# Optimization experiments

Hardware: AMD Instinct MI355X
Metric: run time of the kernel (lower is better)

Reference implementation:

```python
import jax, jax.numpy as jnp
import numpy as np

H = 256  # hidden_dim


def _bidir_lstm_layer(x, W_ih, W_hh, bias):
    """x: [S, B, in]; W_ih: [2, in, 4H]; W_hh: [2, H, 4H]; bias: [2, 4H].
    Returns [S, B, 2H] (forward || backward outputs per timestep).
    PyTorch gate order: i, f, g, o."""
    B = x.shape[1]
    init = (jnp.zeros((B, H), x.dtype), jnp.zeros((B, H), x.dtype))
    # precompute input projections for the whole sequence, both directions
    xp = jnp.einsum('sbi,dij->dsbj', x, W_ih) + bias[:, None, None, :]  # [2,S,B,4H]

    def make_step(W_hh_d):
        def step(carry, xt):
            h, c = carry
            g = xt + h @ W_hh_d  # [B, 4H]
            i = jax.nn.sigmoid(g[:, :H])
            f = jax.nn.sigmoid(g[:, H:2 * H])
            gg = jnp.tanh(g[:, 2 * H:3 * H])
            o = jax.nn.sigmoid(g[:, 3 * H:])
            c = f * c + i * gg
            h = o * jnp.tanh(c)
            return (h, c), h
        return step

    _, h_f = jax.lax.scan(make_step(W_hh[0]), init, xp[0])
    _, h_b = jax.lax.scan(make_step(W_hh[1]), init, xp[1], reverse=True)
    return jnp.concatenate([h_f, h_b], axis=-1)  # [S, B, 2H]


def setup_inputs() -> dict:
    key = jax.random.key(0)
    ks = jax.random.split(key, 11)
    s = 0.05  # small init scale to keep gates in their dynamic range
    inp = {
        'x': jax.random.normal(ks[0], (8192, 1024), jnp.float32),
        'w_ih0': jax.random.normal(ks[1], (2, 1024, 4 * H), jnp.float32) * s,
        'w_hh0': jax.random.normal(ks[2], (2, H, 4 * H), jnp.float32) * s,
        'b0': jax.random.normal(ks[3], (2, 4 * H), jnp.float32) * s,
        'w_ih': jax.random.normal(ks[4], (4, 2, 2 * H, 4 * H), jnp.float32) * s,
        'w_hh': jax.random.normal(ks[5], (4, 2, H, 4 * H), jnp.float32) * s,
        'b': jax.random.normal(ks[6], (4, 2, 4 * H), jnp.float32) * s,
        'w1': jax.random.normal(ks[7], (2 * H, 32), jnp.float32) * s,
        'b1': jax.random.normal(ks[8], (32,), jnp.float32) * s,
        'w2': jax.random.normal(ks[9], (32, 2), jnp.float32) * s,
        'b2': jax.random.normal(ks[10], (2,), jnp.float32) * s,
    }
    return inp


def reference(x, w_ih0, w_hh0, b0, w_ih, w_hh, b, w1, b1, w2, b2):
    # x: [S, 1024] -> [S, B=1, 1024] (module does unsqueeze(0).transpose(0,1))
    h = x[:, None, :]
    h = _bidir_lstm_layer(h, w_ih0, w_hh0, b0)
    for l in range(4):  # layers 1..4 (fixed count)
        h = _bidir_lstm_layer(h, w_ih[l], w_hh[l], b[l])
    # cat(forward output at last step, backward output at first step)
    feat = jnp.concatenate([h[-1, :, :H], h[0, :, H:]], axis=1)  # [1, 2H]
    out = (feat @ w1 + b1) @ w2 + b2  # [1, 2]
    return out
```

## Files before the change

kernel.cpp:

```cpp
#include <hip/hip_runtime.h>

constexpr int SQ = 8192;
constexpr int HD = 256;
constexpr int NG = 1024;

typedef __fp16 h2 __attribute__((ext_vector_type(2)));
typedef __fp16 f16x8 __attribute__((ext_vector_type(8)));
typedef float f32x4 __attribute__((ext_vector_type(4)));
typedef unsigned int uint;
typedef unsigned short ushort;

__device__ __forceinline__ float sigm_f(float x) {
  float e = __builtin_amdgcn_exp2f(-1.4426950408889634f * x);
  return __builtin_amdgcn_rcpf(1.0f + e);
}
__device__ __forceinline__ float tanh_f(float x) {
  float e = __builtin_amdgcn_exp2f(2.885390081777927f * x);
  return 1.0f - 2.0f * __builtin_amdgcn_rcpf(1.0f + e);
}
__device__ __forceinline__ h2 bch2(uint v) { return __builtin_bit_cast(h2, v); }
__device__ __forceinline__ uint pk(float a, float b) {
  return __builtin_bit_cast(uint, __builtin_amdgcn_cvt_pkrtz(a, b));
}
__device__ __forceinline__ f16x8 bcf(uint4 v) { return __builtin_bit_cast(f16x8, v); }
__device__ __forceinline__ float dpp_xor1(float x) {
  int v = __builtin_amdgcn_mov_dpp(__builtin_bit_cast(int, x), 0xB1, 0xF, 0xF, true);
  return __builtin_bit_cast(float, v);
}

__global__ __launch_bounds__(256) void gemm_mfma(const float* __restrict__ A, int K,
                                                 const float* __restrict__ W,
                                                 const float* __restrict__ bias,
                                                 float* __restrict__ out) {
  __shared__ __fp16 Ahi[64][40];
  __shared__ __fp16 Alo[64][40];
  __shared__ __fp16 Bhi[64][40];
  __shared__ __fp16 Blo[64][40];
  const int tid = threadIdx.x;
  const int w   = tid >> 6;
  const int l   = tid & 63;
  const int bm  = blockIdx.x * 64;
  const int d   = blockIdx.y >> 4;
  const int bn  = (blockIdx.y & 15) * 64;
  const float* Wd = W + (size_t)d * K * NG;
  const float* bd = bias + (size_t)d * NG;
  float* outd = out + (size_t)d * SQ * NG;

  const int ar = tid >> 2, ac8 = (tid & 3) * 8;
  const int br = tid >> 3, bc8 = (tid & 7) * 8;

  f32x4 c[4] = {{0.f, 0.f, 0.f, 0.f}, {0.f, 0.f, 0.f, 0.f},
                {0.f, 0.f, 0.f, 0.f}, {0.f, 0.f, 0.f, 0.f}};

  for (int kt = 0; kt < K; kt += 32) {
    float4 a0 = *(const float4*)(A + (size_t)(bm + ar) * K + kt + ac8);
    float4 a1 = *(const float4*)(A + (size_t)(bm + ar) * K + kt + ac8 + 4);
    float4 b0 = *(const float4*)(Wd + (size_t)(kt + br) * NG + bn + bc8);
    float4 b1 = *(const float4*)(Wd + (size_t)(kt + br) * NG + bn + bc8 + 4);
    __syncthreads();
    {
      float av[8] = {a0.x, a0.y, a0.z, a0.w, a1.x, a1.y, a1.z, a1.w};
      __fp16 hi[8], lo[8];
#pragma unroll
      for (int i = 0; i < 8; ++i) {
        hi[i] = (__fp16)av[i];
        lo[i] = (__fp16)(av[i] - (float)hi[i]);
      }
      *(uint4*)&Ahi[ar][ac8] = *(const uint4*)hi;
      *(uint4*)&Alo[ar][ac8] = *(const uint4*)lo;
    }
    {
      float bv[8] = {b0.x, b0.y, b0.z, b0.w, b1.x, b1.y, b1.z, b1.w};
#pragma unroll
      for (int i = 0; i < 8; ++i) {
        __fp16 hi = (__fp16)bv[i];
        Bhi[bc8 + i][br] = hi;
        Blo[bc8 + i][br] = (__fp16)(bv[i] - (float)hi);
      }
    }
    __syncthreads();
    f16x8 ah = bcf(*(const uint4*)&Ahi[w * 16 + (l & 15)][(l >> 4) * 8]);
    f16x8 al = bcf(*(const uint4*)&Alo[w * 16 + (l & 15)][(l >> 4) * 8]);
#pragma unroll
    for (int nt = 0; nt < 4; ++nt) {
      f16x8 bh = bcf(*(const uint4*)&Bhi[nt * 16 + (l & 15)][(l >> 4) * 8]);
      f16x8 bl = bcf(*(const uint4*)&Blo[nt * 16 + (l & 15)][(l >> 4) * 8]);
      c[nt] = __builtin_amdgcn_mfma_f32_16x16x32_f16(ah, bh, c[nt], 0, 0, 0);
      c[nt] = __builtin_amdgcn_mfma_f32_16x16x32_f16(al, bh, c[nt], 0, 0, 0);
      c[nt] = __builtin_amdgcn_mfma_f32_16x16x32_f16(ah, bl, c[nt], 0, 0, 0);
    }
  }

#pragma unroll
  for (int nt = 0; nt < 4; ++nt) {
    const int col = bn + nt * 16 + (l & 15);
    const float bb = bd[col];
#pragma unroll
    for (int r = 0; r < 4; ++r) {
      const int row = bm + w * 16 + (l >> 4) * 4 + r;
      outd[(size_t)row * NG + col] = c[nt][r] + bb;
    }
  }
}

__global__ __launch_bounds__(512, 1) void lstm_rec12(const float* __restrict__ Whh,
                                                     const float* __restrict__ xp,
                                                     float* __restrict__ obuf) {
  __shared__ uint4 wl[16 * 512];
  __shared__ uint  hl[2][128];
  const int d = blockIdx.x;
  const int j = threadIdx.x;
  const int u = j >> 1;
  const int s = j & 1;
  const float* W   = Whh + (size_t)d * HD * NG;
  const float* xpd = xp + (size_t)d * SQ * NG;

  for (int idx = j; idx < 16 * 512; idx += 512) {
    const int rem = idx & 511;
    const int uu  = rem >> 1;
    const int ss  = rem & 1;
    const int qq  = (idx >> 9) & 3;
    const int g   = idx >> 11;
    const int r0  = ss * 128 + 96 + 8 * qq;
    const int c   = g * 256 + uu;
    uint4 v;
    v.x = pk(W[(size_t)(r0 + 0) * NG + c], W[(size_t)(r0 + 1) * NG + c]);
    v.y = pk(W[(size_t)(r0 + 2) * NG + c], W[(size_t)(r0 + 3) * NG + c]);
    v.z = pk(W[(size_t)(r0 + 4) * NG + c], W[(size_t)(r0 + 5) * NG + c]);
    v.w = pk(W[(size_t)(r0 + 6) * NG + c], W[(size_t)(r0 + 7) * NG + c]);
    wl[idx] = v;
  }

  h2 wr[4][48];
#pragma unroll
  for (int g = 0; g < 4; ++g) {
    const float* Wc = W + (size_t)(s * 128) * NG + g * 256 + u;
#pragma unroll
    for (int k = 0; k < 48; ++k)
      wr[g][k] = __builtin_amdgcn_cvt_pkrtz(Wc[(size_t)(2 * k) * NG],
                                            Wc[(size_t)(2 * k + 1) * NG]);
  }

  if (j < 256) { ((uint*)hl)[j] = 0u; }
  __syncthreads();

  const int fwd = (d == 0) ? 1 : 0;
  int t = fwd ? 0 : SQ - 1;
  const int dt = fwd ? 1 : -1;
  float cc = 0.0f;
  int p = 0;

  float xc[4], xn[4] = {};
#pragma unroll
  for (int g = 0; g < 4; ++g) xc[g] = xpd[(size_t)t * NG + g * 256 + u];

  for (int step = 0; step < SQ; ++step) {
    if (step + 1 < SQ) {
#pragma unroll
      for (int g = 0; g < 4; ++g) xn[g] = xpd[(size_t)(t + dt) * NG + g * 256 + u];
    }

    const uint4* hb = (const uint4*)&hl[p][s * 64];
    float acc[4] = {0.0f, 0.0f, 0.0f, 0.0f};
#pragma unroll
    for (int q = 0; q < 12; ++q) {
      uint4 hq = hb[q];
      h2 hx = bch2(hq.x), hy = bch2(hq.y), hz = bch2(hq.z), hw = bch2(hq.w);
#pragma unroll
      for (int g = 0; g < 4; ++g) {
        acc[g] = __builtin_amdgcn_fdot2(wr[g][4 * q + 0], hx, acc[g], false);
        acc[g] = __builtin_amdgcn_fdot2(wr[g][4 * q + 1], hy, acc[g], false);
        acc[g] = __builtin_amdgcn_fdot2(wr[g][4 * q + 2], hz, acc[g], false);
        acc[g] = __builtin_amdgcn_fdot2(wr[g][4 * q + 3], hw, acc[g], false);
      }
    }
#pragma unroll
    for (int qq = 0; qq < 4; ++qq) {
      uint4 hq = hb[12 + qq];
      h2 hx = bch2(hq.x), hy = bch2(hq.y), hz = bch2(hq.z), hw = bch2(hq.w);
#pragma unroll
      for (int g = 0; g < 4; ++g) {
        uint4 wq = wl[(g * 4 + qq) * 512 + j];
        acc[g] = __builtin_amdgcn_fdot2(bch2(wq.x), hx, acc[g], false);
        acc[g] = __builtin_amdgcn_fdot2(bch2(wq.y), hy, acc[g], false);
        acc[g] = __builtin_amdgcn_fdot2(bch2(wq.z), hz, acc[g], false);
        acc[g] = __builtin_amdgcn_fdot2(bch2(wq.w), hw, acc[g], false);
      }
    }

#pragma unroll
    for (int g = 0; g < 4; ++g) acc[g] += dpp_xor1(acc[g]);

    float iv = sigm_f(acc[0] + xc[0]);
    float fv = sigm_f(acc[1] + xc[1]);
    float gv = tanh_f(acc[2] + xc[2]);
    float ov = sigm_f(acc[3] + xc[3]);
    cc = fv * cc + iv * gv;
    float hv = ov * tanh_f(cc);

    if (s == 0) {
      obuf[(size_t)t * 512 + (d << 8) + u] = hv;
      ((ushort*)hl[p ^ 1])[u] = (ushort)(pk(hv, hv) & 0xFFFFu);
    }

    asm volatile("s_waitcnt lgkmcnt(0)" ::: "memory");
    __builtin_amdgcn_s_barrier();
    __builtin_amdgcn_sched_barrier(0);

    p ^= 1;
#pragma unroll
    for (int g = 0; g < 4; ++g) xc[g] = xn[g];
    t += dt;
  }
}

__global__ void cls_k(const float* __restrict__ buf, const float* __restrict__ w1,
                      const float* __restrict__ b1, const float* __restrict__ w2,
                      const float* __restrict__ b2, float* __restrict__ out) {
  __shared__ float feat[512];
  __shared__ float hid[32];
  const int t = threadIdx.x;
  feat[t] = (t < 256) ? buf[(size_t)(SQ - 1) * 512 + t] : buf[t];
  __syncthreads();
  if (t < 32) {
    float a = b1[t];
    for (int k = 0; k < 512; ++k) a = fmaf(feat[k], w1[k * 32 + t], a);
    hid[t] = a;
  }
  __syncthreads();
  if (t < 2) {
    float a = b2[t];
    for (int k = 0; k < 32; ++k) a = fmaf(hid[k], w2[k * 2 + t], a);
    out[t] = a;
  }
}

extern "C" void kernel_launch(void* const* d_in, const int* in_sizes, int n_in,
                              void* d_out, int out_size, void* d_ws, size_t ws_size,
                              hipStream_t stream) {
  const float* x     = (const float*)d_in[0];
  const float* w_ih0 = (const float*)d_in[1];
  const float* w_hh0 = (const float*)d_in[2];
  const float* b0    = (const float*)d_in[3];
  const float* w_ih  = (const float*)d_in[4];
  const float* w_hh  = (const float*)d_in[5];
  const float* b     = (const float*)d_in[6];
  const float* w1    = (const float*)d_in[7];
  const float* b1    = (const float*)d_in[8];
  const float* w2    = (const float*)d_in[9];
  const float* b2    = (const float*)d_in[10];

  float* xp   = (float*)d_ws;
  float* bufA = xp + (size_t)2 * SQ * NG;
  float* bufB = bufA + (size_t)SQ * 512;

  const dim3 ggrid(SQ / 64, 32);

  gemm_mfma<<<ggrid, 256, 0, stream>>>(x, 1024, w_ih0, b0, xp);
  lstm_rec12<<<2, 512, 0, stream>>>(w_hh0, xp, bufA);

  float* cur = bufA;
  float* nxt = bufB;
  for (int lyr = 0; lyr < 4; ++lyr) {
    gemm_mfma<<<ggrid, 256, 0, stream>>>(cur, 512, w_ih + (size_t)lyr * 2 * 512 * 1024,
                                         b + (size_t)lyr * 2 * 1024, xp);
    lstm_rec12<<<2, 512, 0, stream>>>(w_hh + (size_t)lyr * 2 * 256 * 1024, xp, nxt);
    float* tmp = cur; cur = nxt; nxt = tmp;
  }

  cls_k<<<1, 512, 0, stream>>>(cur, w1, b1, w2, b2, (float*)d_out);
}
```

Baseline: 63.25 ms.

## Split LSTM recurrence between MFMA waves and fdot2 waves per block

```diff
diff --git a/kernel.cpp b/kernel.cpp
--- a/kernel.cpp
+++ b/kernel.cpp
@@ -103,104 +103,195 @@
   }
 }
 
-__global__ __launch_bounds__(512, 1) void lstm_rec12(const float* __restrict__ Whh,
-                                                     const float* __restrict__ xp,
-                                                     float* __restrict__ obuf) {
-  __shared__ uint4 wl[16 * 512];
+#define FRAGQ(b) bcf(make_uint4(wregd[(b)], wregd[(b) + 1], wregd[(b) + 2], wregd[(b) + 3]))
+
+__global__ __launch_bounds__(512, 1) void lstm_hyb(const float* __restrict__ Whh,
+                                                   const float* __restrict__ xp,
+                                                   float* __restrict__ obuf) {
+  __shared__ uint4 wlA[16 * 256];
+  __shared__ uint4 wlV[16 * 256];
   __shared__ uint  hl[2][128];
   const int d = blockIdx.x;
   const int j = threadIdx.x;
-  const int u = j >> 1;
-  const int s = j & 1;
+  const int w = j >> 6;
+  const int l = j & 63;
   const float* W   = Whh + (size_t)d * HD * NG;
   const float* xpd = xp + (size_t)d * SQ * NG;
 
-  for (int idx = j; idx < 16 * 512; idx += 512) {
-    const int rem = idx & 511;
-    const int uu  = rem >> 1;
-    const int ss  = rem & 1;
-    const int qq  = (idx >> 9) & 3;
-    const int g   = idx >> 11;
-    const int r0  = ss * 128 + 96 + 8 * qq;
-    const int c   = g * 256 + uu;
-    uint4 v;
-    v.x = pk(W[(size_t)(r0 + 0) * NG + c], W[(size_t)(r0 + 1) * NG + c]);
-    v.y = pk(W[(size_t)(r0 + 2) * NG + c], W[(size_t)(r0 + 3) * NG + c]);
-    v.z = pk(W[(size_t)(r0 + 4) * NG + c], W[(size_t)(r0 + 5) * NG + c]);
-    v.w = pk(W[(size_t)(r0 + 6) * NG + c], W[(size_t)(r0 + 7) * NG + c]);
-    wl[idx] = v;
-  }
-
-  h2 wr[4][48];
-#pragma unroll
-  for (int g = 0; g < 4; ++g) {
-    const float* Wc = W + (size_t)(s * 128) * NG + g * 256 + u;
-#pragma unroll
-    for (int k = 0; k < 48; ++k)
-      wr[g][k] = __builtin_amdgcn_cvt_pkrtz(Wc[(size_t)(2 * k) * NG],
-                                            Wc[(size_t)(2 * k + 1) * NG]);
-  }
-
-  if (j < 256) { ((uint*)hl)[j] = 0u; }
+  const int col16 = l & 15;
+  const int g4 = l >> 4;
+  const int m = w;
+  const int u0 = m * 32 + col16, u1 = u0 + 16;
+  const int jv = j & 255;
+  const int uv = 128 + (jv >> 1);
+  const int s  = jv & 1;
+
+  uint wregd[192];
+  const int fwd = (d == 0) ? 1 : 0;
+  const int t0 = fwd ? 0 : SQ - 1;
+  const int dt = fwd ? 1 : -1;
+  float xc[8], xn[8] = {};
+
+  if (w < 4) {
+#pragma unroll
+    for (int c = 0; c < 6; ++c) {
+      const int colb = (c >> 1) * 256 + m * 32 + (c & 1) * 16 + col16;
+#pragma unroll
+      for (int ks = 0; ks < 8; ++ks) {
+        const int r0 = ks * 32 + g4 * 8;
+        const int b = (c * 8 + ks) * 4;
+        wregd[b + 0] = pk(W[(size_t)(r0 + 0) * NG + colb], W[(size_t)(r0 + 1) * NG + colb]);
+        wregd[b + 1] = pk(W[(size_t)(r0 + 2) * NG + colb], W[(size_t)(r0 + 3) * NG + colb]);
+        wregd[b + 2] = pk(W[(size_t)(r0 + 4) * NG + colb], W[(size_t)(r0 + 5) * NG + colb]);
+        wregd[b + 3] = pk(W[(size_t)(r0 + 6) * NG + colb], W[(size_t)(r0 + 7) * NG + colb]);
+      }
+    }
+#pragma unroll
+    for (int c6 = 0; c6 < 2; ++c6) {
+      const int colb = 768 + m * 32 + c6 * 16 + col16;
+#pragma unroll
+      for (int ks = 0; ks < 8; ++ks) {
+        const int r0 = ks * 32 + g4 * 8;
+        uint4 v;
+        v.x = pk(W[(size_t)(r0 + 0) * NG + colb], W[(size_t)(r0 + 1) * NG + colb]);
+        v.y = pk(W[(size_t)(r0 + 2) * NG + colb], W[(size_t)(r0 + 3) * NG + colb]);
+        v.z = pk(W[(size_t)(r0 + 4) * NG + colb], W[(size_t)(r0 + 5) * NG + colb]);
+        v.w = pk(W[(size_t)(r0 + 6) * NG + colb], W[(size_t)(r0 + 7) * NG + colb]);
+        wlA[(c6 * 8 + ks) * 256 + m * 64 + l] = v;
+      }
+    }
+#pragma unroll
+    for (int c = 0; c < 8; ++c)
+      xc[c] = xpd[(size_t)t0 * NG + (c >> 1) * 256 + m * 32 + (c & 1) * 16 + col16];
+  } else {
+#pragma unroll
+    for (int g = 0; g < 4; ++g) {
+      const float* Wc = W + (size_t)(s * 128) * NG + g * 256 + uv;
+#pragma unroll
+      for (int k = 0; k < 48; ++k)
+        wregd[g * 48 + k] = pk(Wc[(size_t)(2 * k) * NG], Wc[(size_t)(2 * k + 1) * NG]);
+    }
+#pragma unroll
+    for (int g = 0; g < 4; ++g) {
+#pragma unroll
+      for (int qq = 0; qq < 4; ++qq) {
+        const int r0 = s * 128 + 96 + 8 * qq;
+        const int c = g * 256 + uv;
+        uint4 v;
+        v.x = pk(W[(size_t)(r0 + 0) * NG + c], W[(size_t)(r0 + 1) * NG + c]);
+        v.y = pk(W[(size_t)(r0 + 2) * NG + c], W[(size_t)(r0 + 3) * NG + c]);
+        v.z = pk(W[(size_t)(r0 + 4) * NG + c], W[(size_t)(r0 + 5) * NG + c]);
+        v.w = pk(W[(size_t)(r0 + 6) * NG + c], W[(size_t)(r0 + 7) * NG + c]);
+        wlV[(g * 4 + qq) * 256 + jv] = v;
+      }
+    }
+#pragma unroll
+    for (int g = 0; g < 4; ++g) xc[g] = xpd[(size_t)t0 * NG + g * 256 + uv];
+  }
+
+  if (j < 256) ((uint*)hl)[j] = 0u;
   __syncthreads();
 
-  const int fwd = (d == 0) ? 1 : 0;
-  int t = fwd ? 0 : SQ - 1;
-  const int dt = fwd ? 1 : -1;
-  float cc = 0.0f;
+  int t = t0;
+  float cc0 = 0.0f, cc1 = 0.0f;
+  float cc  = 0.0f;
   int p = 0;
 
-  float xc[4], xn[4] = {};
-#pragma unroll
-  for (int g = 0; g < 4; ++g) xc[g] = xpd[(size_t)t * NG + g * 256 + u];
-
   for (int step = 0; step < SQ; ++step) {
-    if (step + 1 < SQ) {
-#pragma unroll
-      for (int g = 0; g < 4; ++g) xn[g] = xpd[(size_t)(t + dt) * NG + g * 256 + u];
-    }
-
-    const uint4* hb = (const uint4*)&hl[p][s * 64];
-    float acc[4] = {0.0f, 0.0f, 0.0f, 0.0f};
-#pragma unroll
-    for (int q = 0; q < 12; ++q) {
-      uint4 hq = hb[q];
-      h2 hx = bch2(hq.x), hy = bch2(hq.y), hz = bch2(hq.z), hw = bch2(hq.w);
-#pragma unroll
-      for (int g = 0; g < 4; ++g) {
-        acc[g] = __builtin_amdgcn_fdot2(wr[g][4 * q + 0], hx, acc[g], false);
-        acc[g] = __builtin_amdgcn_fdot2(wr[g][4 * q + 1], hy, acc[g], false);
-        acc[g] = __builtin_amdgcn_fdot2(wr[g][4 * q + 2], hz, acc[g], false);
-        acc[g] = __builtin_amdgcn_fdot2(wr[g][4 * q + 3], hw, acc[g], false);
-      }
-    }
-#pragma unroll
-    for (int qq = 0; qq < 4; ++qq) {
-      uint4 hq = hb[12 + qq];
-      h2 hx = bch2(hq.x), hy = bch2(hq.y), hz = bch2(hq.z), hw = bch2(hq.w);
-#pragma unroll
-      for (int g = 0; g < 4; ++g) {
-        uint4 wq = wl[(g * 4 + qq) * 512 + j];
-        acc[g] = __builtin_amdgcn_fdot2(bch2(wq.x), hx, acc[g], false);
-        acc[g] = __builtin_amdgcn_fdot2(bch2(wq.y), hy, acc[g], false);
-        acc[g] = __builtin_amdgcn_fdot2(bch2(wq.z), hz, acc[g], false);
-        acc[g] = __builtin_amdgcn_fdot2(bch2(wq.w), hw, acc[g], false);
-      }
-    }
-
-#pragma unroll
-    for (int g = 0; g < 4; ++g) acc[g] += dpp_xor1(acc[g]);
-
-    float iv = sigm_f(acc[0] + xc[0]);
-    float fv = sigm_f(acc[1] + xc[1]);
-    float gv = tanh_f(acc[2] + xc[2]);
-    float ov = sigm_f(acc[3] + xc[3]);
-    cc = fv * cc + iv * gv;
-    float hv = ov * tanh_f(cc);
-
-    if (s == 0) {
-      obuf[(size_t)t * 512 + (d << 8) + u] = hv;
-      ((ushort*)hl[p ^ 1])[u] = (ushort)(pk(hv, hv) & 0xFFFFu);
+    if (w < 4) {
+      if (step + 1 < SQ) {
+#pragma unroll
+        for (int c = 0; c < 8; ++c)
+          xn[c] = xpd[(size_t)(t + dt) * NG + (c >> 1) * 256 + m * 32 + (c & 1) * 16 + col16];
+      }
+      float pre[8];
+      {
+        f32x4 c0 = {0.f, 0.f, 0.f, 0.f}, c1 = c0, c2 = c0, c3 = c0;
+#pragma unroll
+        for (int ks = 0; ks < 8; ++ks) {
+          f16x8 a = bcf(*(const uint4*)&hl[p][ks * 16 + g4 * 4]);
+          c0 = __builtin_amdgcn_mfma_f32_16x16x32_f16(a, FRAGQ((0 * 8 + ks) * 4), c0, 0, 0, 0);
+          c1 = __builtin_amdgcn_mfma_f32_16x16x32_f16(a, FRAGQ((1 * 8 + ks) * 4), c1, 0, 0, 0);
+          c2 = __builtin_amdgcn_mfma_f32_16x16x32_f16(a, FRAGQ((2 * 8 + ks) * 4), c2, 0, 0, 0);
+          c3 = __builtin_amdgcn_mfma_f32_16x16x32_f16(a, FRAGQ((3 * 8 + ks) * 4), c3, 0, 0, 0);
+        }
+        pre[0] = c0[0]; pre[1] = c1[0]; pre[2] = c2[0]; pre[3] = c3[0];
+      }
+      {
+        f32x4 c0 = {0.f, 0.f, 0.f, 0.f}, c1 = c0, c2 = c0, c3 = c0;
+#pragma unroll
+        for (int ks = 0; ks < 8; ++ks) {
+          f16x8 a = bcf(*(const uint4*)&hl[p][ks * 16 + g4 * 4]);
+          c0 = __builtin_amdgcn_mfma_f32_16x16x32_f16(a, FRAGQ((4 * 8 + ks) * 4), c0, 0, 0, 0);
+          c1 = __builtin_amdgcn_mfma_f32_16x16x32_f16(a, FRAGQ((5 * 8 + ks) * 4), c1, 0, 0, 0);
+          c2 = __builtin_amdgcn_mfma_f32_16x16x32_f16(a, bcf(wlA[(0 * 8 + ks) * 256 + m * 64 + l]), c2, 0, 0, 0);
+          c3 = __builtin_amdgcn_mfma_f32_16x16x32_f16(a, bcf(wlA[(1 * 8 + ks) * 256 + m * 64 + l]), c3, 0, 0, 0);
+        }
+        pre[4] = c0[0]; pre[5] = c1[0]; pre[6] = c2[0]; pre[7] = c3[0];
+      }
+      float i0 = sigm_f(pre[0] + xc[0]);
+      float i1 = sigm_f(pre[1] + xc[1]);
+      float f0 = sigm_f(pre[2] + xc[2]);
+      float f1 = sigm_f(pre[3] + xc[3]);
+      float g0 = tanh_f(pre[4] + xc[4]);
+      float g1 = tanh_f(pre[5] + xc[5]);
+      float o0 = sigm_f(pre[6] + xc[6]);
+      float o1 = sigm_f(pre[7] + xc[7]);
+      cc0 = f0 * cc0 + i0 * g0;
+      cc1 = f1 * cc1 + i1 * g1;
+      float hv0 = o0 * tanh_f(cc0);
+      float hv1 = o1 * tanh_f(cc1);
+      if (l < 16) {
+        obuf[(size_t)t * 512 + (d << 8) + u0] = hv0;
+        obuf[(size_t)t * 512 + (d << 8) + u1] = hv1;
+        ushort* hp = (ushort*)hl[p ^ 1];
+        hp[u0] = (ushort)(pk(hv0, hv0) & 0xFFFFu);
+        hp[u1] = (ushort)(pk(hv1, hv1) & 0xFFFFu);
+      }
+    } else {
+      if (step + 1 < SQ) {
+#pragma unroll
+        for (int g = 0; g < 4; ++g) xn[g] = xpd[(size_t)(t + dt) * NG + g * 256 + uv];
+      }
+      const uint4* hb = (const uint4*)&hl[p][s * 64];
+      float acc[4] = {0.0f, 0.0f, 0.0f, 0.0f};
+#pragma unroll
+      for (int q = 0; q < 12; ++q) {
+        uint4 hq = hb[q];
+        h2 hx = bch2(hq.x), hy = bch2(hq.y), hz = bch2(hq.z), hw = bch2(hq.w);
+#pragma unroll
+        for (int g = 0; g < 4; ++g) {
+          acc[g] = __builtin_amdgcn_fdot2(bch2(wregd[g * 48 + 4 * q + 0]), hx, acc[g], false);
+          acc[g] = __builtin_amdgcn_fdot2(bch2(wregd[g * 48 + 4 * q + 1]), hy, acc[g], false);
+          acc[g] = __builtin_amdgcn_fdot2(bch2(wregd[g * 48 + 4 * q + 2]), hz, acc[g], false);
+          acc[g] = __builtin_amdgcn_fdot2(bch2(wregd[g * 48 + 4 * q + 3]), hw, acc[g], false);
+        }
+      }
+#pragma unroll
+      for (int qq = 0; qq < 4; ++qq) {
+        uint4 hq = hb[12 + qq];
+        h2 hx = bch2(hq.x), hy = bch2(hq.y), hz = bch2(hq.z), hw = bch2(hq.w);
+#pragma unroll
+        for (int g = 0; g < 4; ++g) {
+          uint4 wq = wlV[(g * 4 + qq) * 256 + jv];
+          acc[g] = __builtin_amdgcn_fdot2(bch2(wq.x), hx, acc[g], false);
+          acc[g] = __builtin_amdgcn_fdot2(bch2(wq.y), hy, acc[g], false);
+          acc[g] = __builtin_amdgcn_fdot2(bch2(wq.z), hz, acc[g], false);
+          acc[g] = __builtin_amdgcn_fdot2(bch2(wq.w), hw, acc[g], false);
+        }
+      }
+#pragma unroll
+      for (int g = 0; g < 4; ++g) acc[g] += dpp_xor1(acc[g]);
+      float iv = sigm_f(acc[0] + xc[0]);
+      float fv = sigm_f(acc[1] + xc[1]);
+      float gv = tanh_f(acc[2] + xc[2]);
+      float ov = sigm_f(acc[3] + xc[3]);
+      cc = fv * cc + iv * gv;
+      float hv = ov * tanh_f(cc);
+      if (s == 0) {
+        obuf[(size_t)t * 512 + (d << 8) + uv] = hv;
+        ((ushort*)hl[p ^ 1])[uv] = (ushort)(pk(hv, hv) & 0xFFFFu);
+      }
     }
 
     asm volatile("s_waitcnt lgkmcnt(0)" ::: "memory");
@@ -209,7 +300,7 @@
 
     p ^= 1;
 #pragma unroll
-    for (int g = 0; g < 4; ++g) xc[g] = xn[g];
+    for (int i = 0; i < 8; ++i) xc[i] = xn[i];
     t += dt;
   }
 }
@@ -257,14 +348,14 @@
   const dim3 ggrid(SQ / 64, 32);
 
   gemm_mfma<<<ggrid, 256, 0, stream>>>(x, 1024, w_ih0, b0, xp);
-  lstm_rec12<<<2, 512, 0, stream>>>(w_hh0, xp, bufA);
+  lstm_hyb<<<2, 512, 0, stream>>>(w_hh0, xp, bufA);
 
   float* cur = bufA;
   float* nxt = bufB;
   for (int lyr = 0; lyr < 4; ++lyr) {
     gemm_mfma<<<ggrid, 256, 0, stream>>>(cur, 512, w_ih + (size_t)lyr * 2 * 512 * 1024,
                                          b + (size_t)lyr * 2 * 1024, xp);
-    lstm_rec12<<<2, 512, 0, stream>>>(w_hh + (size_t)lyr * 2 * 256 * 1024, xp, nxt);
+    lstm_hyb<<<2, 512, 0, stream>>>(w_hh + (size_t)lyr * 2 * 256 * 1024, xp, nxt);
     float* tmp = cur; cur = nxt; nxt = tmp;
   }
 
```

After: 106.3 ms. +68.1%, slower.
